# Kernel optimization log

Hardware: AMD Instinct MI355X
Metric: run time of the kernel (lower is better)

Reference implementation:

```python
import jax, jax.numpy as jnp
import numpy as np

B, S, D = 16, 577, 768
H = 12
DH = D // H  # 64


def setup_inputs() -> dict:
    key = jax.random.key(0)
    ks = jax.random.split(key, 7)
    s = 0.02
    return {
        "hidden_states": jax.random.normal(ks[0], (B, S, D), dtype=jnp.float32),
        "wq": jax.random.normal(ks[1], (D, D), dtype=jnp.float32) * s,
        "bq": jnp.zeros((D,), dtype=jnp.float32),
        "wk": jax.random.normal(ks[2], (D, D), dtype=jnp.float32) * s,
        "bk": jnp.zeros((D,), dtype=jnp.float32),
        "wv": jax.random.normal(ks[3], (D, D), dtype=jnp.float32) * s,
        "bv": jnp.zeros((D,), dtype=jnp.float32),
    }


def reference(hidden_states, wq, bq, wk, bk, wv, bv):
    # Linear projections (torch nn.Linear: x @ W^T + b)
    q = hidden_states @ wq.T + bq  # [B,S,D]
    k = hidden_states @ wk.T + bk
    v = hidden_states @ wv.T + bv

    def split_heads(x):
        return x.reshape(B, S, H, DH).transpose(0, 2, 1, 3)  # [B,H,S,DH]

    q, k, v = split_heads(q), split_heads(k), split_heads(v)
    scale = 1.0 / jnp.sqrt(jnp.float32(DH))
    scores = jnp.einsum("bhqd,bhkd->bhqk", q, k) * scale  # [B,H,S,S]
    probs = jax.nn.softmax(scores, axis=-1)
    ctx = jnp.einsum("bhqk,bhkd->bhqd", probs, v)  # [B,H,S,DH]
    ctx = ctx.transpose(0, 2, 1, 3).reshape(B, S, D)
    return ctx, probs
```

## Files before the change

kernel.cpp:

```cpp
#include <hip/hip_runtime.h>
#include <hip/hip_bf16.h>
#include <cstdint>

#define B_  16
#define S_  577
#define D_  768
#define H_  12
#define SP  640
#define M_  (B_*S_)
#define MP  9344
#define N_  2304
#define SCS 664
#define QSCALE 0.18033688011112042f

typedef __attribute__((ext_vector_type(8))) short short8;
typedef __attribute__((ext_vector_type(4))) float f32x4;
typedef unsigned int u32;

static __device__ __forceinline__ unsigned short f2bf(float f) {
    __bf16 b = (__bf16)f;
    return __builtin_bit_cast(unsigned short, b);
}
static __device__ __forceinline__ u32 cvtpk(float lo, float hi) {
    return (u32)f2bf(lo) | ((u32)f2bf(hi) << 16);
}
static __device__ __forceinline__ float bf2f(unsigned short u) {
    uint32_t x = ((uint32_t)u) << 16;
    return __builtin_bit_cast(float, x);
}
static __device__ __forceinline__ float exp2_raw(float x) {
    float r;
    asm("v_exp_f32 %0, %1" : "=v"(r) : "v"(x));
    return r;
}

typedef __attribute__((address_space(3))) u32 lds_u32;
typedef __attribute__((address_space(1))) const u32 gbl_u32;
static __device__ __forceinline__ void gll16(const void* g, void* l) {
    __builtin_amdgcn_global_load_lds((gbl_u32*)g, (lds_u32*)l, 16, 0, 0);
}


__global__ __launch_bounds__(256) void prep(
    const float* __restrict__ X,
    const float* __restrict__ Wq, const float* __restrict__ Wk, const float* __restrict__ Wv,
    unsigned short* __restrict__ Xb, unsigned short* __restrict__ Wb,
    unsigned short* __restrict__ Vf)
{
    const int NT1 = MP * 192;
    const int NT2 = N_ * 192;
    const int VPAD = 192 * 1024;
    const int total = NT1 + NT2 + VPAD;
    const int stride = gridDim.x * 256;
    for (int i = blockIdx.x * 256 + threadIdx.x; i < total; i += stride) {
        if (i < NT1) {
            int row = i / 192, c4 = i - row * 192;
            uint2 out = make_uint2(0u, 0u);
            if (row < M_) {
                float4 v = *(const float4*)(X + (size_t)row * 768 + c4 * 4);
                out.x = cvtpk(v.x, v.y); out.y = cvtpk(v.z, v.w);
            }
            *(uint2*)(Xb + (size_t)row * 768 + c4 * 4) = out;
        } else if (i < NT1 + NT2) {
            int j = i - NT1;
            int row = j / 192, c4 = j - row * 192;
            const float* src = (row < 768) ? (Wq + (size_t)row * 768)
                             : (row < 1536) ? (Wk + (size_t)(row - 768) * 768)
                                            : (Wv + (size_t)(row - 1536) * 768);
            float4 v = *(const float4*)(src + c4 * 4);
            uint2 out;
            out.x = cvtpk(v.x, v.y); out.y = cvtpk(v.z, v.w);
            *(uint2*)(Wb + (size_t)row * 768 + c4 * 4) = out;
        } else {
            int j = i - NT1 - NT2;
            int bh = j >> 10, rem = j & 1023;
            *(uint2*)(Vf + (size_t)bh * 40960 + 36864 + rem * 4) = make_uint2(0u, 0u);
        }
    }
}

__global__ __launch_bounds__(256) void qkv_gemm(
    const unsigned short* __restrict__ Xb, const unsigned short* __restrict__ Wb,
    const float* __restrict__ bq, const float* __restrict__ bk, const float* __restrict__ bv,
    unsigned short* __restrict__ Qf, unsigned short* __restrict__ Kf,
    unsigned short* __restrict__ Vf)
{
    __shared__ unsigned short Als[128 * 64];
    __shared__ unsigned short Bls[128 * 64];

    const int bid = blockIdx.x;
    int mt, nt;
    if (bid < 1296) {
        const int xcd = bid & 7, sq = bid >> 3;
        mt = xcd * 9 + sq / 18;
        nt = sq % 18;
    } else {
        mt = 72;
        nt = bid - 1296;
    }

    const bool qk = (nt < 12);
    const int tid = threadIdx.x, lane = tid & 63, wid = tid >> 6;
    const int wm = wid >> 1, wn = wid & 1;
    const int m0 = mt * 128, n0 = nt * 128;
    const int l15 = lane & 15, g = lane >> 4;
    const int prow = lane >> 3, pc8 = lane & 7;

    const unsigned short* Pa = qk ? Bls : Als;
    const unsigned short* Pb = qk ? Als : Bls;

    f32x4 acc[4][4] = {};

    for (int kk = 0; kk < 768; kk += 64) {
        __syncthreads();
        #pragma unroll
        for (int t = 0; t < 4; ++t) {
            int row  = wid * 32 + t * 8 + prow;
            int scol = ((pc8 ^ (row & 7)) * 8);
            gll16(Xb + (size_t)(m0 + row) * 768 + kk + scol, &Als[(wid * 32 + t * 8) * 64]);
            gll16(Wb + (size_t)(n0 + row) * 768 + kk + scol, &Bls[(wid * 32 + t * 8) * 64]);
        }
        __syncthreads();

        #pragma unroll
        for (int ks = 0; ks < 2; ++ks) {
            short8 fa[4], fb[4];
            #pragma unroll
            for (int i = 0; i < 4; ++i) {
                int row = wm * 64 + i * 16 + l15;
                fa[i] = *(const short8*)&Pa[row * 64 + (((ks * 4 + g) ^ (row & 7)) * 8)];
            }
            #pragma unroll
            for (int j = 0; j < 4; ++j) {
                int row = wn * 64 + j * 16 + l15;
                fb[j] = *(const short8*)&Pb[row * 64 + (((ks * 4 + g) ^ (row & 7)) * 8)];
            }
            #pragma unroll
            for (int i = 0; i < 4; ++i)
                #pragma unroll
                for (int j = 0; j < 4; ++j)
                    acc[i][j] = __builtin_amdgcn_mfma_f32_16x16x32_bf16(fa[i], fb[j], acc[i][j], 0, 0, 0);
        }
    }

    if (qk) {
        const float* bb = (nt < 6) ? bq : bk;
        unsigned short* Dst = (nt < 6) ? Qf : Kf;
        const float scale = (nt < 6) ? QSCALE : 1.0f;
        const int n0p = n0 - ((nt < 6) ? 0 : 768);

        float4 b4[4]; int Pi[4];
        #pragma unroll
        for (int i = 0; i < 4; ++i) {
            int nrow0 = n0p + wm * 64 + i * 16 + g * 4;
            b4[i] = *(const float4*)(bb + nrow0);
            int hh = nrow0 >> 6, d0 = nrow0 & 63;
            int base = (d0 >> 5) * 512 + ((d0 >> 3) & 3) * 8 + (d0 & 7);
            Pi[i] = ((nt < 6) ? hh * 1024 : hh * 40960) + base;
        }
        #pragma unroll
        for (int j = 0; j < 4; ++j) {
            int m = m0 + wn * 64 + j * 16 + l15;
            if (m >= M_) continue;
            int b = m / 577, s = m - b * 577;
            int Pj = (nt < 6)
                   ? b * 491520 + (s >> 4) * 12288 + (s & 15) * 32
                   : b * 491520 + (s >> 6) * 4096 + ((s >> 4) & 3) * 1024 + (s & 15) * 32;
            #pragma unroll
            for (int i = 0; i < 4; ++i) {
                uint2 p;
                p.x = cvtpk((acc[i][j][0] + b4[i].x) * scale, (acc[i][j][1] + b4[i].y) * scale);
                p.y = cvtpk((acc[i][j][2] + b4[i].z) * scale, (acc[i][j][3] + b4[i].w) * scale);
                *(uint2*)(Dst + Pj + Pi[i]) = p;
            }
        }
    } else {
        int Pir[4][4]; bool mv[4][4];
        #pragma unroll
        for (int i = 0; i < 4; ++i) {
            int mi = m0 + wm * 64 + i * 16 + g * 4;
            int b = mi / 577, s = mi - b * 577;
            #pragma unroll
            for (int r = 0; r < 4; ++r) {
                int bb2 = b, ss = s + r;
                if (ss >= 577) { bb2++; ss -= 577; }
                mv[i][r] = (mi + r < M_);
                Pir[i][r] = bb2 * 491520 + (ss >> 5) * 2048 + ((ss >> 3) & 3) * 8 + (ss & 7);
            }
        }
        #pragma unroll
        for (int j = 0; j < 4; ++j) {
            int nn = n0 + wn * 64 + j * 16 + l15 - 1536;
            float bias = bv[nn];
            int hh = nn >> 6, dwh = nn & 63;
            int Pn = hh * 40960 + (dwh >> 4) * 512 + (dwh & 15) * 32;
            #pragma unroll
            for (int i = 0; i < 4; ++i)
                #pragma unroll
                for (int r = 0; r < 4; ++r)
                    if (mv[i][r])
                        Vf[Pn + Pir[i][r]] = f2bf(acc[i][j][r] + bias);
        }
    }
}

__global__ __launch_bounds__(256) void attn(
    const unsigned short* __restrict__ Qf, const unsigned short* __restrict__ Kf,
    const unsigned short* __restrict__ Vf,
    float* __restrict__ ctx, float* __restrict__ probs)
{
    __shared__ unsigned short sc[16 * SCS];
    __shared__ float rowinv[16];

    const int wg  = blockIdx.x;
    const int idx = (wg & 7) * 888 + (wg >> 3);
    const int bh  = idx / 37;
    const int qt  = idx - bh * 37;
    const int h   = bh % 12, b = bh / 12;

    const int tid = threadIdx.x, lane = tid & 63, wid = tid >> 6;
    const int l15 = lane & 15, g = lane >> 4;
    const int q0 = qt * 16;
    const int lofs = l15 * 32 + g * 8;
    const int r = tid >> 4, c0 = tid & 15;

    const unsigned short* qb = Qf + ((size_t)(b * 40 + qt) * 12 + h) * 1024 + lofs;
    short8 aq0 = *(const short8*)qb;
    short8 aq1 = *(const short8*)(qb + 512);

    const unsigned short* kb0 = Kf + (size_t)bh * 40960 + wid * 1024 + lofs;
    short8 kr0[10], kr1[10];
    #pragma unroll
    for (int c = 0; c < 10; ++c) {
        const unsigned short* kb = kb0 + c * 4096;
        kr0[c] = *(const short8*)kb;
        kr1[c] = *(const short8*)(kb + 512);
    }
    #pragma unroll
    for (int c = 0; c < 10; ++c) {
        f32x4 s4 = {};
        s4 = __builtin_amdgcn_mfma_f32_16x16x32_bf16(aq0, kr0[c], s4, 0, 0, 0);
        s4 = __builtin_amdgcn_mfma_f32_16x16x32_bf16(aq1, kr1[c], s4, 0, 0, 0);
        int key = c * 64 + wid * 16 + l15;
        #pragma unroll
        for (int rr = 0; rr < 4; ++rr)
            sc[(g * 4 + rr) * SCS + key] = (key < S_) ? f2bf(s4[rr]) : (unsigned short)0xFF80u;
    }
    __syncthreads();

    unsigned short* rowp = &sc[r * SCS];
    float inv;
    {
        float m = -1e30f;
        #pragma unroll
        for (int i = 0; i < 5; ++i) {
            short8 v = *(const short8*)&rowp[(c0 + 16 * i) * 8];
            float t0 = fmaxf(bf2f((unsigned short)v[0]), bf2f((unsigned short)v[1]));
            float t1 = fmaxf(bf2f((unsigned short)v[2]), bf2f((unsigned short)v[3]));
            float t2 = fmaxf(bf2f((unsigned short)v[4]), bf2f((unsigned short)v[5]));
            float t3 = fmaxf(bf2f((unsigned short)v[6]), bf2f((unsigned short)v[7]));
            m = fmaxf(m, fmaxf(fmaxf(t0, t1), fmaxf(t2, t3)));
        }
        #pragma unroll
        for (int o = 8; o; o >>= 1) m = fmaxf(m, __shfl_xor(m, o));

        float ssum = 0.f;
        #pragma unroll
        for (int i = 0; i < 5; ++i) {
            short8 v = *(const short8*)&rowp[(c0 + 16 * i) * 8];
            float e0 = exp2_raw(bf2f((unsigned short)v[0]) - m);
            float e1 = exp2_raw(bf2f((unsigned short)v[1]) - m);
            float e2 = exp2_raw(bf2f((unsigned short)v[2]) - m);
            float e3 = exp2_raw(bf2f((unsigned short)v[3]) - m);
            float e4 = exp2_raw(bf2f((unsigned short)v[4]) - m);
            float e5 = exp2_raw(bf2f((unsigned short)v[5]) - m);
            float e6 = exp2_raw(bf2f((unsigned short)v[6]) - m);
            float e7 = exp2_raw(bf2f((unsigned short)v[7]) - m);
            uint4 w;
            w.x = cvtpk(e0, e1); w.y = cvtpk(e2, e3);
            w.z = cvtpk(e4, e5); w.w = cvtpk(e6, e7);
            *(uint4*)&rowp[(c0 + 16 * i) * 8] = w;
            ssum += ((e0 + e1) + (e2 + e3)) + ((e4 + e5) + (e6 + e7));
        }
        #pragma unroll
        for (int o = 8; o; o >>= 1) ssum += __shfl_xor(ssum, o);
        inv = 1.0f / ssum;
        if (c0 == 0) rowinv[r] = inv;
    }
    __syncthreads();

    const unsigned short* vb0 = Vf + (size_t)bh * 40960 + wid * 512 + lofs;
    short8 vr0[10], vr1[10];
    #pragma unroll
    for (int kk = 0; kk < 10; ++kk) {
        vr0[kk] = *(const short8*)(vb0 + (size_t)(2 * kk) * 2048);
        vr1[kk] = *(const short8*)(vb0 + (size_t)(2 * kk + 1) * 2048);
    }

    {
        int q = q0 + r;
        if (q < S_) {
            float* prow = probs + ((size_t)bh * S_ + q) * S_;
            #pragma unroll
            for (int i = 0; i < 5; ++i) {
                int ch = c0 + 16 * i;
                short8 v = *(const short8*)&rowp[ch * 8];
                if (ch < 72) {
                    f32x4 o0, o1;
                    o0[0] = bf2f((unsigned short)v[0]) * inv; o0[1] = bf2f((unsigned short)v[1]) * inv;
                    o0[2] = bf2f((unsigned short)v[2]) * inv; o0[3] = bf2f((unsigned short)v[3]) * inv;
                    o1[0] = bf2f((unsigned short)v[4]) * inv; o1[1] = bf2f((unsigned short)v[5]) * inv;
                    o1[2] = bf2f((unsigned short)v[6]) * inv; o1[3] = bf2f((unsigned short)v[7]) * inv;
                    __builtin_nontemporal_store(o0, (f32x4*)&prow[ch * 8]);
                    __builtin_nontemporal_store(o1, (f32x4*)&prow[ch * 8 + 4]);
                } else if (ch == 72) {
                    __builtin_nontemporal_store(bf2f((unsigned short)v[0]) * inv, &prow[576]);
                }
            }
        }
    }

    f32x4 oc0 = {}, oc1 = {};
    const unsigned short* pb = &sc[l15 * SCS + g * 8];
    #pragma unroll
    for (int kk = 0; kk < 10; ++kk) {
        short8 ap0 = *(const short8*)(pb + (2 * kk) * 32);
        oc0 = __builtin_amdgcn_mfma_f32_16x16x32_bf16(ap0, vr0[kk], oc0, 0, 0, 0);
        short8 ap1 = *(const short8*)(pb + (2 * kk + 1) * 32);
        oc1 = __builtin_amdgcn_mfma_f32_16x16x32_bf16(ap1, vr1[kk], oc1, 0, 0, 0);
    }
    f32x4 oc = oc0 + oc1;
    #pragma unroll
    for (int rr = 0; rr < 4; ++rr) {
        int qr = g * 4 + rr;
        int qq = q0 + qr;
        if (qq < S_)
            __builtin_nontemporal_store(oc[rr] * rowinv[qr],
                &ctx[((size_t)b * S_ + qq) * D_ + h * 64 + wid * 16 + l15]);
    }
}

extern "C" void kernel_launch(void* const* d_in, const int* in_sizes, int n_in,
                              void* d_out, int out_size, void* d_ws, size_t ws_size,
                              hipStream_t stream) {
    const float* X  = (const float*)d_in[0];
    const float* Wq = (const float*)d_in[1];
    const float* bq = (const float*)d_in[2];
    const float* Wk = (const float*)d_in[3];
    const float* bk = (const float*)d_in[4];
    const float* Wv = (const float*)d_in[5];
    const float* bv = (const float*)d_in[6];

    float* ctx   = (float*)d_out;
    float* probs = ctx + (size_t)B_ * S_ * D_;

    unsigned short* Xb = (unsigned short*)probs;
    unsigned short* Wb = Xb + (size_t)MP * 768;

    unsigned short* Qf = (unsigned short*)d_ws;
    unsigned short* Kf = Qf + (size_t)7864320;
    unsigned short* Vf = Kf + (size_t)7864320;

    prep<<<dim3(1024), 256, 0, stream>>>(X, Wq, Wk, Wv, Xb, Wb, Vf);
    qkv_gemm<<<dim3(1314), 256, 0, stream>>>(Xb, Wb, bq, bk, bv, Qf, Kf, Vf);
    attn<<<dim3(7104), 256, 0, stream>>>(Qf, Kf, Vf, ctx, probs);
}
```

Measured before the change: 197.0 us.

## Double-buffer QKV GEMM LDS tiles and use 8 waves per block

The QKV projection GEMM now keeps two LDS buffers for its A and B tiles, so the next K-slice is prefetched while the current one is computed, and only one barrier is needed per iteration. The block grows from 256 to 512 threads (8 waves in a 2x4 layout), and each wave now owns a 64x32 output subtile, which halves the accumulator registers per wave. The aim is to hide global-load latency and raise MFMA issue density. The cost is double the LDS per block, which may reduce the number of resident blocks.

```diff
diff --git a/kernel.cpp b/kernel.cpp
--- a/kernel.cpp
+++ b/kernel.cpp
@@ -79,14 +79,14 @@
     }
 }
 
-__global__ __launch_bounds__(256) void qkv_gemm(
+__global__ __launch_bounds__(512) void qkv_gemm(
     const unsigned short* __restrict__ Xb, const unsigned short* __restrict__ Wb,
     const float* __restrict__ bq, const float* __restrict__ bk, const float* __restrict__ bv,
     unsigned short* __restrict__ Qf, unsigned short* __restrict__ Kf,
     unsigned short* __restrict__ Vf)
 {
-    __shared__ unsigned short Als[128 * 64];
-    __shared__ unsigned short Bls[128 * 64];
+    __shared__ unsigned short Als[2][128 * 64];
+    __shared__ unsigned short Bls[2][128 * 64];
 
     const int bid = blockIdx.x;
     int mt, nt;
@@ -101,47 +101,64 @@
 
     const bool qk = (nt < 12);
     const int tid = threadIdx.x, lane = tid & 63, wid = tid >> 6;
-    const int wm = wid >> 1, wn = wid & 1;
+    const int wm = wid >> 2, wn = wid & 3;
     const int m0 = mt * 128, n0 = nt * 128;
     const int l15 = lane & 15, g = lane >> 4;
     const int prow = lane >> 3, pc8 = lane & 7;
 
-    const unsigned short* Pa = qk ? Bls : Als;
-    const unsigned short* Pb = qk ? Als : Bls;
-
-    f32x4 acc[4][4] = {};
-
-    for (int kk = 0; kk < 768; kk += 64) {
+    f32x4 acc[4][2] = {};
+
+    #define STAGE(buf, kkarg)                                                           \
+        {                                                                               \
+            _Pragma("unroll")                                                           \
+            for (int tt2 = 0; tt2 < 2; ++tt2) {                                         \
+                int row  = wid * 16 + tt2 * 8 + prow;                                   \
+                int scol = ((pc8 ^ (row & 7)) * 8);                                     \
+                gll16(Xb + (size_t)(m0 + row) * 768 + (kkarg) + scol,                   \
+                      &Als[buf][(wid * 16 + tt2 * 8) * 64]);                            \
+                gll16(Wb + (size_t)(n0 + row) * 768 + (kkarg) + scol,                   \
+                      &Bls[buf][(wid * 16 + tt2 * 8) * 64]);                            \
+            }                                                                           \
+        }
+
+    #define COMPUTE(buf)                                                                \
+        {                                                                               \
+            const unsigned short* PA = qk ? Bls[buf] : Als[buf];                        \
+            const unsigned short* PB = qk ? Als[buf] : Bls[buf];                        \
+            _Pragma("unroll")                                                           \
+            for (int ks = 0; ks < 2; ++ks) {                                            \
+                short8 fa[4], fb[2];                                                    \
+                _Pragma("unroll")                                                       \
+                for (int i = 0; i < 4; ++i) {                                           \
+                    int row = wm * 64 + i * 16 + l15;                                   \
+                    fa[i] = *(const short8*)&PA[row * 64 + (((ks * 4 + g) ^ (row & 7)) * 8)]; \
+                }                                                                       \
+                _Pragma("unroll")                                                       \
+                for (int j = 0; j < 2; ++j) {                                           \
+                    int row = wn * 32 + j * 16 + l15;                                   \
+                    fb[j] = *(const short8*)&PB[row * 64 + (((ks * 4 + g) ^ (row & 7)) * 8)]; \
+                }                                                                       \
+                _Pragma("unroll")                                                       \
+                for (int i = 0; i < 4; ++i)                                             \
+                    _Pragma("unroll")                                                   \
+                    for (int j = 0; j < 2; ++j)                                         \
+                        acc[i][j] = __builtin_amdgcn_mfma_f32_16x16x32_bf16(            \
+                            fa[i], fb[j], acc[i][j], 0, 0, 0);                          \
+            }                                                                           \
+        }
+
+    STAGE(0, 0);
+    __syncthreads();
+    int cur = 0;
+    #pragma unroll 1
+    for (int t = 0; t < 12; ++t) {
+        if (t < 11) STAGE(cur ^ 1, (t + 1) * 64);
+        COMPUTE(cur);
         __syncthreads();
-        #pragma unroll
-        for (int t = 0; t < 4; ++t) {
-            int row  = wid * 32 + t * 8 + prow;
-            int scol = ((pc8 ^ (row & 7)) * 8);
-            gll16(Xb + (size_t)(m0 + row) * 768 + kk + scol, &Als[(wid * 32 + t * 8) * 64]);
-            gll16(Wb + (size_t)(n0 + row) * 768 + kk + scol, &Bls[(wid * 32 + t * 8) * 64]);
-        }
-        __syncthreads();
-
-        #pragma unroll
-        for (int ks = 0; ks < 2; ++ks) {
-            short8 fa[4], fb[4];
-            #pragma unroll
-            for (int i = 0; i < 4; ++i) {
-                int row = wm * 64 + i * 16 + l15;
-                fa[i] = *(const short8*)&Pa[row * 64 + (((ks * 4 + g) ^ (row & 7)) * 8)];
-            }
-            #pragma unroll
-            for (int j = 0; j < 4; ++j) {
-                int row = wn * 64 + j * 16 + l15;
-                fb[j] = *(const short8*)&Pb[row * 64 + (((ks * 4 + g) ^ (row & 7)) * 8)];
-            }
-            #pragma unroll
-            for (int i = 0; i < 4; ++i)
-                #pragma unroll
-                for (int j = 0; j < 4; ++j)
-                    acc[i][j] = __builtin_amdgcn_mfma_f32_16x16x32_bf16(fa[i], fb[j], acc[i][j], 0, 0, 0);
-        }
-    }
+        cur ^= 1;
+    }
+    #undef STAGE
+    #undef COMPUTE
 
     if (qk) {
         const float* bb = (nt < 6) ? bq : bk;
@@ -159,8 +176,8 @@
             Pi[i] = ((nt < 6) ? hh * 1024 : hh * 40960) + base;
         }
         #pragma unroll
-        for (int j = 0; j < 4; ++j) {
-            int m = m0 + wn * 64 + j * 16 + l15;
+        for (int j = 0; j < 2; ++j) {
+            int m = m0 + wn * 32 + j * 16 + l15;
             if (m >= M_) continue;
             int b = m / 577, s = m - b * 577;
             int Pj = (nt < 6)
@@ -189,8 +206,8 @@
             }
         }
         #pragma unroll
-        for (int j = 0; j < 4; ++j) {
-            int nn = n0 + wn * 64 + j * 16 + l15 - 1536;
+        for (int j = 0; j < 2; ++j) {
+            int nn = n0 + wn * 32 + j * 16 + l15 - 1536;
             float bias = bv[nn];
             int hh = nn >> 6, dwh = nn & 63;
             int Pn = hh * 40960 + (dwh >> 4) * 512 + (dwh & 15) * 32;
@@ -362,6 +379,6 @@
     unsigned short* Vf = Kf + (size_t)7864320;
 
     prep<<<dim3(1024), 256, 0, stream>>>(X, Wq, Wk, Wv, Xb, Wb, Vf);
-    qkv_gemm<<<dim3(1314), 256, 0, stream>>>(Xb, Wb, bq, bk, bv, Qf, Kf, Vf);
+    qkv_gemm<<<dim3(1314), 512, 0, stream>>>(Xb, Wb, bq, bk, bv, Qf, Kf, Vf);
     attn<<<dim3(7104), 256, 0, stream>>>(Qf, Kf, Vf, ctx, probs);
 }
```

Measured after the change: 182.0 us. 7.6% less time.
